# Performance work log

Measured on AMD Instinct MI355X. Metric: run time of the kernel, lower is better.

## Reference

```python
import jax, jax.numpy as jnp
import numpy as np
import math

D_MODEL = 1024
HEADS = 16
HEAD_DIM = D_MODEL // HEADS
B, S = 2, 2048


def setup_inputs() -> dict:
    key = jax.random.key(0)
    ks = jax.random.split(key, 7)
    scale = 1.0 / math.sqrt(D_MODEL)
    return {
        "query": jax.random.normal(ks[0], (B, S, D_MODEL), dtype=jnp.float32),
        "key": jax.random.normal(ks[1], (B, S, D_MODEL), dtype=jnp.float32),
        "value": jax.random.normal(ks[2], (B, S, D_MODEL), dtype=jnp.float32),
        # causal mask, broadcast over batch and heads: [1, 1, S, S]
        "mask": jnp.tril(jnp.ones((S, S), dtype=bool))[None, None],
        "Wq": jax.random.normal(ks[3], (D_MODEL, D_MODEL), dtype=jnp.float32) * scale,
        "Wk": jax.random.normal(ks[4], (D_MODEL, D_MODEL), dtype=jnp.float32) * scale,
        "Wv": jax.random.normal(ks[5], (D_MODEL, D_MODEL), dtype=jnp.float32) * scale,
        "Wo": jax.random.normal(ks[6], (D_MODEL, D_MODEL), dtype=jnp.float32) * scale,
    }


def reference(query, key, value, mask, Wq, Wk, Wv, Wo):
    # bias-free projections (nn.Linear: x @ W.T)
    q = query @ Wq.T  # [B, S, D]
    k = key @ Wk.T
    v = value @ Wv.T

    def split_heads(x):  # [B, S, D] -> [B, H, S, Dh]
        return x.reshape(B, -1, HEADS, HEAD_DIM).transpose(0, 2, 1, 3)

    q, k, v = split_heads(q), split_heads(k), split_heads(v)

    # scores: [B, H, S, S]
    scores = jnp.einsum("bhsd,bhtd->bhst", q, k) / math.sqrt(HEAD_DIM)
    scores = jnp.where(mask, scores, -1e9)
    attn = jax.nn.softmax(scores, axis=-1)
    # dropout omitted (eval-mode reference; p=0.1 in training)
    out = jnp.einsum("bhst,bhtd->bhsd", attn, v)  # [B, H, S, Dh]
    out = out.transpose(0, 2, 1, 3).reshape(B, -1, D_MODEL)
    return out @ Wo.T
```

## Files before the change

kernel.cpp:

```cpp
#include <hip/hip_runtime.h>

#define BATCH 2
#define SEQ   2048
#define DMODEL 1024
#define NHEADS 16
#define HDIM  64

typedef __attribute__((ext_vector_type(8))) short short8v;
typedef __attribute__((ext_vector_type(4))) float f32x4;
typedef unsigned int uint32;

__device__ __forceinline__ unsigned short bf16rne(float x) {
    uint32 u = __float_as_uint(x);
    return (unsigned short)((u + 0x7FFFu + ((u >> 16) & 1u)) >> 16);
}
__device__ __forceinline__ void split1(float x, unsigned short& h, unsigned short& l) {
    uint32 u = __float_as_uint(x);
    uint32 hb = (u + 0x7FFFu + ((u >> 16) & 1u)) & 0xFFFF0000u;
    h = (unsigned short)(hb >> 16);
    float r = x - __uint_as_float(hb);
    l = bf16rne(r);
}

__global__ __launch_bounds__(256)
void cvt_hi3(const float* __restrict__ s0, const float* __restrict__ s1,
             const float* __restrict__ s2, short* __restrict__ d0,
             short* __restrict__ d1, short* __restrict__ d2, int n) {
    const float* src; short* dst;
    if (blockIdx.y == 0)      { src = s0; dst = d0; }
    else if (blockIdx.y == 1) { src = s1; dst = d1; }
    else                      { src = s2; dst = d2; }
    int i = (blockIdx.x * 256 + threadIdx.x) * 4;
    if (i >= n) return;
    float4 x = *reinterpret_cast<const float4*>(src + i);
    *reinterpret_cast<ushort4*>(dst + i) =
        make_ushort4(bf16rne(x.x), bf16rne(x.y), bf16rne(x.z), bf16rne(x.w));
}

__global__ __launch_bounds__(256)
void split_hl(const float* __restrict__ src, short* __restrict__ hi,
              short* __restrict__ lo, int n) {
    int i = (blockIdx.x * 256 + threadIdx.x) * 4;
    if (i >= n) return;
    float4 x = *reinterpret_cast<const float4*>(src + i);
    unsigned short h0, h1, h2, h3, l0, l1, l2, l3;
    split1(x.x, h0, l0); split1(x.y, h1, l1);
    split1(x.z, h2, l2); split1(x.w, h3, l3);
    *reinterpret_cast<ushort4*>(hi + i) = make_ushort4(h0, h1, h2, h3);
    *reinterpret_cast<ushort4*>(lo + i) = make_ushort4(l0, l1, l2, l3);
}

__device__ __forceinline__ void gload_lds16(const void* g, void* l) {
    __builtin_amdgcn_global_load_lds((const __attribute__((address_space(1))) void*)g,
                                     (__attribute__((address_space(3))) void*)l,
                                     16, 0, 0);
}

__global__ __launch_bounds__(256)
void gemm_qkv_bf16(const short* __restrict__ aq, const short* __restrict__ ak,
                   const short* __restrict__ av,
                   const short* __restrict__ wq, const short* __restrict__ wk,
                   const short* __restrict__ wv,
                   short* __restrict__ qo, short* __restrict__ ko,
                   short* __restrict__ vo) {
    __shared__ short As[128 * 64];
    __shared__ short Bs[128 * 64];
    const int tid = threadIdx.x;
    const int lane = tid & 63;
    const int w = tid >> 6, wm = w >> 1, wn = w & 1;
    const int r = lane & 15, g = lane >> 4;

    int soff[4];
    #pragma unroll
    for (int c = 0; c < 4; ++c) {
        const int u = c * 256 + tid, row = u >> 3, s = u & 7;
        soff[c] = row * 1024 + ((s ^ (row & 7)) * 8);
    }

    const int z = blockIdx.z;
    const short* A; const short* B; int bm, bn;
    if (z == 0)      { A = aq; B = wq; bm = blockIdx.y * 128; bn = blockIdx.x * 128; }
    else if (z == 1) { A = ak; B = wk; bm = blockIdx.y * 128; bn = blockIdx.x * 128; }
    else             { A = wv; B = av; bm = blockIdx.x * 128; bn = blockIdx.y * 128; }

    f32x4 acc[4][4];
    #pragma unroll
    for (int i = 0; i < 4; ++i)
        #pragma unroll
        for (int j = 0; j < 4; ++j) acc[i][j] = (f32x4){0.f, 0.f, 0.f, 0.f};

    const short* Arow = A + (size_t)bm * 1024;
    const short* Brow = B + (size_t)bn * 1024;
    for (int k0 = 0; k0 < 1024; k0 += 64) {
        __syncthreads();
        #pragma unroll
        for (int c = 0; c < 4; ++c) {
            gload_lds16(Arow + k0 + soff[c], &As[(c * 256 + tid) * 8]);
            gload_lds16(Brow + k0 + soff[c], &Bs[(c * 256 + tid) * 8]);
        }
        __syncthreads();
        #pragma unroll
        for (int kk = 0; kk < 2; ++kk) {
            short8v af[4], bf[4];
            #pragma unroll
            for (int fm = 0; fm < 4; ++fm)
                af[fm] = *(const short8v*)&As[(wm * 64 + fm * 16 + r) * 64 +
                                              (((kk * 4 + g) ^ (r & 7))) * 8];
            #pragma unroll
            for (int fn = 0; fn < 4; ++fn)
                bf[fn] = *(const short8v*)&Bs[(wn * 64 + fn * 16 + r) * 64 +
                                              (((kk * 4 + g) ^ (r & 7))) * 8];
            #pragma unroll
            for (int fm = 0; fm < 4; ++fm)
                #pragma unroll
                for (int fn = 0; fn < 4; ++fn)
                    acc[fm][fn] = __builtin_amdgcn_mfma_f32_16x16x32_bf16(
                        af[fm], bf[fn], acc[fm][fn], 0, 0, 0);
        }
    }

    #pragma unroll
    for (int fm = 0; fm < 4; ++fm)
        #pragma unroll
        for (int fn = 0; fn < 4; ++fn)
            #pragma unroll
            for (int qi = 0; qi < 4; ++qi) {
                const int mrow = bm + wm * 64 + fm * 16 + g * 4 + qi;
                const int ncol = bn + wn * 64 + fn * 16 + r;
                const float v = acc[fm][fn][qi];
                if (z == 0) {
                    size_t idx = ((size_t)((mrow >> 11) * 16 + (ncol >> 6))) * (SEQ * 64)
                               + (size_t)(mrow & 2047) * 64 + (ncol & 63);
                    qo[idx] = (short)bf16rne(v * 0.125f);
                } else if (z == 1) {
                    size_t idx = ((size_t)((mrow >> 11) * 16 + (ncol >> 6))) * (SEQ * 64)
                               + (size_t)(mrow & 2047) * 64 + (ncol & 63);
                    ko[idx] = (short)bf16rne(v);
                } else {
                    size_t idx = ((size_t)((ncol >> 11) * 16 + (mrow >> 6))) * (SEQ * 64)
                               + (size_t)(mrow & 63) * SEQ + (ncol & 2047);
                    vo[idx] = (short)bf16rne(v);
                }
            }
}

__device__ __forceinline__ void gemm512_pass(const short* __restrict__ Arow,
                                             const short* __restrict__ Brow,
                                             short* As, short* Bs,
                                             f32x4 (&acc)[4][2], int tid) {
    const int lane = tid & 63;
    const int w = tid >> 6, wm = w >> 2, wn = w & 3;
    const int r = lane & 15, g = lane >> 4;
    int soff[2];
    #pragma unroll
    for (int c = 0; c < 2; ++c) {
        const int u = c * 512 + tid, row = u >> 3, s = u & 7;
        soff[c] = row * 1024 + ((s ^ (row & 7)) * 8);
    }
    for (int k0 = 0; k0 < 1024; k0 += 64) {
        __syncthreads();
        #pragma unroll
        for (int c = 0; c < 2; ++c) {
            gload_lds16(Arow + k0 + soff[c], &As[(c * 512 + tid) * 8]);
            gload_lds16(Brow + k0 + soff[c], &Bs[(c * 512 + tid) * 8]);
        }
        __syncthreads();
        #pragma unroll
        for (int kk = 0; kk < 2; ++kk) {
            short8v af[4], bf[2];
            #pragma unroll
            for (int fm = 0; fm < 4; ++fm)
                af[fm] = *(const short8v*)&As[(wm * 64 + fm * 16 + r) * 64 +
                                              (((kk * 4 + g) ^ (r & 7))) * 8];
            #pragma unroll
            for (int fn = 0; fn < 2; ++fn)
                bf[fn] = *(const short8v*)&Bs[(wn * 32 + fn * 16 + r) * 64 +
                                              (((kk * 4 + g) ^ (r & 7))) * 8];
            #pragma unroll
            for (int fm = 0; fm < 4; ++fm)
                #pragma unroll
                for (int fn = 0; fn < 2; ++fn)
                    acc[fm][fn] = __builtin_amdgcn_mfma_f32_16x16x32_bf16(
                        af[fm], bf[fn], acc[fm][fn], 0, 0, 0);
        }
    }
}

__global__ __launch_bounds__(512)
void gemm_out_f32(const short* __restrict__ Ah, const short* __restrict__ Al,
                  const short* __restrict__ Bh, const short* __restrict__ Bl,
                  float* __restrict__ C) {
    __shared__ short As[128 * 64];
    __shared__ short Bs[128 * 64];
    const int tid = threadIdx.x;
    const int bm = blockIdx.y * 128, bn = blockIdx.x * 128;

    f32x4 acc[4][2];
    #pragma unroll
    for (int i = 0; i < 4; ++i)
        #pragma unroll
        for (int j = 0; j < 2; ++j) acc[i][j] = (f32x4){0.f, 0.f, 0.f, 0.f};

    gemm512_pass(Ah + (size_t)bm * 1024, Bh + (size_t)bn * 1024, As, Bs, acc, tid);
    gemm512_pass(Ah + (size_t)bm * 1024, Bl + (size_t)bn * 1024, As, Bs, acc, tid);
    gemm512_pass(Al + (size_t)bm * 1024, Bh + (size_t)bn * 1024, As, Bs, acc, tid);

    const int lane = tid & 63;
    const int w = tid >> 6, wm = w >> 2, wn = w & 3;
    const int r = lane & 15, g = lane >> 4;
    #pragma unroll
    for (int fm = 0; fm < 4; ++fm)
        #pragma unroll
        for (int fn = 0; fn < 2; ++fn)
            #pragma unroll
            for (int qi = 0; qi < 4; ++qi) {
                const int mrow = bm + wm * 64 + fm * 16 + g * 4 + qi;
                const int ncol = bn + wn * 32 + fn * 16 + r;
                C[(size_t)mrow * DMODEL + ncol] = acc[fm][fn][qi];
            }
}

__global__ __launch_bounds__(256, 3)
void attn_split(const short* __restrict__ qh, const short* __restrict__ kh,
                const short* __restrict__ vt, short* __restrict__ oh,
                short* __restrict__ ol) {
    __shared__ short Pl[4][32 * 64];
    __shared__ float Ls[4][32];
    const int tid  = threadIdx.x;
    const int lane = tid & 63;
    const int wid  = tid >> 6;
    const int r = lane & 15;
    const int g = lane >> 4;
    const int c  = 63 - (int)blockIdx.x;
    const int bh = blockIdx.y;
    short* Pw = Pl[wid];
    float* Ob = reinterpret_cast<float*>(&Pl[0][0]);

    const short* qB = qh + (size_t)bh * SEQ * 64;
    const short* kB = kh + (size_t)bh * SEQ * 64;
    const short* vB = vt + (size_t)bh * 64 * SEQ;
    const int b = bh >> 4, h = bh & 15;
    const int q0 = c * 32;
    const int nt = (c + 2) >> 1;

    short8v qf[2][2];
    #pragma unroll
    for (int fm = 0; fm < 2; ++fm)
        #pragma unroll
        for (int kk = 0; kk < 2; ++kk)
            qf[fm][kk] = *(const short8v*)(qB + (size_t)(q0 + fm * 16 + r) * 64 +
                                           (kk * 4 + g) * 8);

    f32x4 oacc[2][4];
    float lsum[2][4];
    #pragma unroll
    for (int fm = 0; fm < 2; ++fm) {
        #pragma unroll
        for (int fd = 0; fd < 4; ++fd) oacc[fm][fd] = (f32x4){0.f, 0.f, 0.f, 0.f};
        #pragma unroll
        for (int qi = 0; qi < 4; ++qi) lsum[fm][qi] = 0.f;
    }

    for (int kt = wid; kt < nt; kt += 4) {
        f32x4 sacc[2][4];
        #pragma unroll
        for (int fm = 0; fm < 2; ++fm)
            #pragma unroll
            for (int fn = 0; fn < 4; ++fn) sacc[fm][fn] = (f32x4){0.f, 0.f, 0.f, 0.f};
        #pragma unroll
        for (int kk = 0; kk < 2; ++kk) {
            short8v kf[4];
            #pragma unroll
            for (int fn = 0; fn < 4; ++fn)
                kf[fn] = *(const short8v*)(kB + (size_t)(kt * 64 + fn * 16 + r) * 64 +
                                           (kk * 4 + g) * 8);
            #pragma unroll
            for (int fm = 0; fm < 2; ++fm)
                #pragma unroll
                for (int fn = 0; fn < 4; ++fn)
                    sacc[fm][fn] = __builtin_amdgcn_mfma_f32_16x16x32_bf16(
                        qf[fm][kk], kf[fn], sacc[fm][fn], 0, 0, 0);
        }

        if (kt == nt - 1) {
            #pragma unroll
            for (int fm = 0; fm < 2; ++fm)
                #pragma unroll
                for (int fn = 0; fn < 4; ++fn)
                    #pragma unroll
                    for (int qi = 0; qi < 4; ++qi) {
                        const int qg = q0 + fm * 16 + g * 4 + qi;
                        const int kg = kt * 64 + fn * 16 + r;
                        if (kg > qg) sacc[fm][fn][qi] = -1.0e30f;
                    }
        }

        #pragma unroll
        for (int fm = 0; fm < 2; ++fm)
            #pragma unroll
            for (int fn = 0; fn < 4; ++fn)
                #pragma unroll
                for (int qi = 0; qi < 4; ++qi) {
                    const float p = __expf(sacc[fm][fn][qi]);
                    sacc[fm][fn][qi] = p;
                    lsum[fm][qi] += p;
                }

        #pragma unroll
        for (int fm = 0; fm < 2; ++fm)
            #pragma unroll
            for (int fn = 0; fn < 4; ++fn)
                #pragma unroll
                for (int qi = 0; qi < 4; ++qi) {
                    const int ql = fm * 16 + g * 4 + qi;
                    const int kl = fn * 16 + r;
                    Pw[ql * 64 + (((kl >> 3) ^ (ql & 7)) << 3) + (kl & 7)] =
                        (short)bf16rne(sacc[fm][fn][qi]);
                }

        #pragma unroll
        for (int kk = 0; kk < 2; ++kk) {
            short8v pf[2], vf[4];
            #pragma unroll
            for (int fm = 0; fm < 2; ++fm)
                pf[fm] = *(const short8v*)&Pw[(fm * 16 + r) * 64 +
                                              (((kk * 4 + g) ^ (r & 7))) * 8];
            #pragma unroll
            for (int fd = 0; fd < 4; ++fd)
                vf[fd] = *(const short8v*)(vB + (size_t)(fd * 16 + r) * SEQ +
                                           kt * 64 + (kk * 4 + g) * 8);
            #pragma unroll
            for (int fm = 0; fm < 2; ++fm)
                #pragma unroll
                for (int fd = 0; fd < 4; ++fd)
                    oacc[fm][fd] = __builtin_amdgcn_mfma_f32_16x16x32_bf16(
                        pf[fm], vf[fd], oacc[fm][fd], 0, 0, 0);
        }
    }

    #pragma unroll
    for (int fm = 0; fm < 2; ++fm)
        #pragma unroll
        for (int qi = 0; qi < 4; ++qi) {
            float s = lsum[fm][qi];
            s += __shfl_xor(s, 1);
            s += __shfl_xor(s, 2);
            s += __shfl_xor(s, 4);
            s += __shfl_xor(s, 8);
            lsum[fm][qi] = s;
        }
    if (r == 0) {
        #pragma unroll
        for (int fm = 0; fm < 2; ++fm)
            #pragma unroll
            for (int qi = 0; qi < 4; ++qi)
                Ls[wid][fm * 16 + g * 4 + qi] = lsum[fm][qi];
    }

    __syncthreads();

    if (wid >= 2) {
        float* dst = Ob + (wid - 2) * 2048;
        #pragma unroll
        for (int fm = 0; fm < 2; ++fm)
            #pragma unroll
            for (int fd = 0; fd < 4; ++fd)
                #pragma unroll
                for (int qi = 0; qi < 4; ++qi)
                    dst[(fm * 16 + g * 4 + qi) * 64 + fd * 16 + r] = oacc[fm][fd][qi];
    }
    __syncthreads();
    if (wid < 2) {
        const float* src = Ob + wid * 2048;
        #pragma unroll
        for (int fm = 0; fm < 2; ++fm)
            #pragma unroll
            for (int fd = 0; fd < 4; ++fd)
                #pragma unroll
                for (int qi = 0; qi < 4; ++qi)
                    oacc[fm][fd][qi] += src[(fm * 16 + g * 4 + qi) * 64 + fd * 16 + r];
    }
    __syncthreads();
    if (wid == 1) {
        #pragma unroll
        for (int fm = 0; fm < 2; ++fm)
            #pragma unroll
            for (int fd = 0; fd < 4; ++fd)
                #pragma unroll
                for (int qi = 0; qi < 4; ++qi)
                    Ob[(fm * 16 + g * 4 + qi) * 64 + fd * 16 + r] = oacc[fm][fd][qi];
    }
    __syncthreads();
    if (wid == 0) {
        #pragma unroll
        for (int fm = 0; fm < 2; ++fm)
            #pragma unroll
            for (int fd = 0; fd < 4; ++fd)
                #pragma unroll
                for (int qi = 0; qi < 4; ++qi)
                    oacc[fm][fd][qi] += Ob[(fm * 16 + g * 4 + qi) * 64 + fd * 16 + r];

        float inv[2][4];
        #pragma unroll
        for (int fm = 0; fm < 2; ++fm)
            #pragma unroll
            for (int qi = 0; qi < 4; ++qi) {
                const int row = fm * 16 + g * 4 + qi;
                inv[fm][qi] = 1.0f / (Ls[0][row] + Ls[1][row] + Ls[2][row] + Ls[3][row]);
            }

        #pragma unroll
        for (int fm = 0; fm < 2; ++fm)
            #pragma unroll
            for (int fd = 0; fd < 4; ++fd)
                #pragma unroll
                for (int qi = 0; qi < 4; ++qi) {
                    const float v = oacc[fm][fd][qi] * inv[fm][qi];
                    unsigned short hh, ll;
                    split1(v, hh, ll);
                    const int mg = b * SEQ + q0 + fm * 16 + g * 4 + qi;
                    const int nc = h * 64 + fd * 16 + r;
                    const size_t idx = (size_t)mg * DMODEL + nc;
                    oh[idx] = (short)hh; ol[idx] = (short)ll;
                }
    }
}

extern "C" void kernel_launch(void* const* d_in, const int* in_sizes, int n_in,
                              void* d_out, int out_size, void* d_ws, size_t ws_size,
                              hipStream_t stream) {
    const float* query = (const float*)d_in[0];
    const float* key   = (const float*)d_in[1];
    const float* value = (const float*)d_in[2];
    const float* Wq = (const float*)d_in[4];
    const float* Wk = (const float*)d_in[5];
    const float* Wv = (const float*)d_in[6];
    const float* Wo = (const float*)d_in[7];
    float* out = (float*)d_out;

    const size_t SD = (size_t)BATCH * SEQ * DMODEL;
    const size_t DD = (size_t)DMODEL * DMODEL;
    const int M = BATCH * SEQ;

    short* ws  = (short*)d_ws;
    short* aq  = ws;
    short* ak  = aq + SD;
    short* av  = ak + SD;
    short* wqh = av + SD;
    short* wkh = wqh + DD;
    short* wvh = wkh + DD;
    short* qh_ = wvh + DD;
    short* kh_ = qh_ + SD;
    short* vt_ = kh_ + SD;
    short* woh = vt_ + SD;
    short* wol = woh + DD;
    short* oh_ = aq;
    short* ol_ = ak;

    dim3 gc_a((unsigned)(SD / 1024), 3);
    cvt_hi3<<<gc_a, 256, 0, stream>>>(query, key, value, aq, ak, av, (int)SD);
    dim3 gc_w((unsigned)(DD / 1024), 3);
    cvt_hi3<<<gc_w, 256, 0, stream>>>(Wq, Wk, Wv, wqh, wkh, wvh, (int)DD);

    dim3 gq(DMODEL / 128, M / 128, 3);
    gemm_qkv_bf16<<<gq, 256, 0, stream>>>(aq, ak, av, wqh, wkh, wvh, qh_, kh_, vt_);

    dim3 ga(64, BATCH * NHEADS);
    attn_split<<<ga, 256, 0, stream>>>(qh_, kh_, vt_, oh_, ol_);

    split_hl<<<(int)(DD / 1024), 256, 0, stream>>>(Wo, woh, wol, (int)DD);

    dim3 go(DMODEL / 128, M / 128);
    gemm_out_f32<<<go, 512, 0, stream>>>(oh_, ol_, woh, wol, out);
}
```

Before: 329.4 us.

## Pair causal query chunks per block and switch softmax exponent to exp2

Each attention block now handles two query chunks, c and 63-c, so every block gets roughly the same causal workload and the grid is halved. Occupancy is raised to 4 blocks per CU, and the first V fragment load is issued before the masking and exp work to hide its latency. The Q projection scale now folds in log2(e), so the softmax can use the hardware exp2 instead of __expf. The catch is more barriers per block, and, as in the code before, no running max is subtracted, which relies on scores staying bounded.

```diff
diff --git a/kernel.cpp b/kernel.cpp
--- a/kernel.cpp
+++ b/kernel.cpp
@@ -20,6 +20,13 @@
     h = (unsigned short)(hb >> 16);
     float r = x - __uint_as_float(hb);
     l = bf16rne(r);
+}
+__device__ __forceinline__ float fexp2(float x) {
+#if __has_builtin(__builtin_amdgcn_exp2f)
+    return __builtin_amdgcn_exp2f(x);
+#else
+    return exp2f(x);
+#endif
 }
 
 __global__ __launch_bounds__(256)
@@ -131,7 +138,7 @@
                 if (z == 0) {
                     size_t idx = ((size_t)((mrow >> 11) * 16 + (ncol >> 6))) * (SEQ * 64)
                                + (size_t)(mrow & 2047) * 64 + (ncol & 63);
-                    qo[idx] = (short)bf16rne(v * 0.125f);
+                    qo[idx] = (short)bf16rne(v * 0.18033688011112043f);
                 } else if (z == 1) {
                     size_t idx = ((size_t)((mrow >> 11) * 16 + (ncol >> 6))) * (SEQ * 64)
                                + (size_t)(mrow & 2047) * 64 + (ncol & 63);
@@ -220,10 +227,10 @@
             }
 }
 
-__global__ __launch_bounds__(256, 3)
-void attn_split(const short* __restrict__ qh, const short* __restrict__ kh,
-                const short* __restrict__ vt, short* __restrict__ oh,
-                short* __restrict__ ol) {
+__global__ __launch_bounds__(256, 4)
+void attn_pair(const short* __restrict__ qh, const short* __restrict__ kh,
+               const short* __restrict__ vt, short* __restrict__ oh,
+               short* __restrict__ ol) {
     __shared__ short Pl[4][32 * 64];
     __shared__ float Ls[4][32];
     const int tid  = threadIdx.x;
@@ -231,7 +238,7 @@
     const int wid  = tid >> 6;
     const int r = lane & 15;
     const int g = lane >> 4;
-    const int c  = 63 - (int)blockIdx.x;
+    const int x  = blockIdx.x;
     const int bh = blockIdx.y;
     short* Pw = Pl[wid];
     float* Ob = reinterpret_cast<float*>(&Pl[0][0]);
@@ -240,189 +247,212 @@
     const short* kB = kh + (size_t)bh * SEQ * 64;
     const short* vB = vt + (size_t)bh * 64 * SEQ;
     const int b = bh >> 4, h = bh & 15;
-    const int q0 = c * 32;
-    const int nt = (c + 2) >> 1;
-
-    short8v qf[2][2];
-    #pragma unroll
-    for (int fm = 0; fm < 2; ++fm)
-        #pragma unroll
-        for (int kk = 0; kk < 2; ++kk)
-            qf[fm][kk] = *(const short8v*)(qB + (size_t)(q0 + fm * 16 + r) * 64 +
-                                           (kk * 4 + g) * 8);
-
-    f32x4 oacc[2][4];
-    float lsum[2][4];
-    #pragma unroll
-    for (int fm = 0; fm < 2; ++fm) {
-        #pragma unroll
-        for (int fd = 0; fd < 4; ++fd) oacc[fm][fd] = (f32x4){0.f, 0.f, 0.f, 0.f};
-        #pragma unroll
-        for (int qi = 0; qi < 4; ++qi) lsum[fm][qi] = 0.f;
-    }
-
-    for (int kt = wid; kt < nt; kt += 4) {
-        f32x4 sacc[2][4];
+
+    #pragma unroll
+    for (int half = 0; half < 2; ++half) {
+        const int c  = half ? (63 - x) : x;
+        const int q0 = c * 32;
+        const int nt = (c + 2) >> 1;
+
+        short8v qf[2][2];
         #pragma unroll
         for (int fm = 0; fm < 2; ++fm)
             #pragma unroll
-            for (int fn = 0; fn < 4; ++fn) sacc[fm][fn] = (f32x4){0.f, 0.f, 0.f, 0.f};
-        #pragma unroll
-        for (int kk = 0; kk < 2; ++kk) {
-            short8v kf[4];
-            #pragma unroll
-            for (int fn = 0; fn < 4; ++fn)
-                kf[fn] = *(const short8v*)(kB + (size_t)(kt * 64 + fn * 16 + r) * 64 +
-                                           (kk * 4 + g) * 8);
-            #pragma unroll
-            for (int fm = 0; fm < 2; ++fm)
+            for (int kk = 0; kk < 2; ++kk)
+                qf[fm][kk] = *(const short8v*)(qB + (size_t)(q0 + fm * 16 + r) * 64 +
+                                               (kk * 4 + g) * 8);
+
+        f32x4 oacc[2][4];
+        float lsum[2][4];
+        #pragma unroll
+        for (int fm = 0; fm < 2; ++fm) {
+            #pragma unroll
+            for (int fd = 0; fd < 4; ++fd) oacc[fm][fd] = (f32x4){0.f, 0.f, 0.f, 0.f};
+            #pragma unroll
+            for (int qi = 0; qi < 4; ++qi) lsum[fm][qi] = 0.f;
+        }
+
+        for (int kt = wid; kt < nt; kt += 4) {
+            f32x4 sacc[2][4];
+            #pragma unroll
+            for (int fm = 0; fm < 2; ++fm)
+                #pragma unroll
+                for (int fn = 0; fn < 4; ++fn) sacc[fm][fn] = (f32x4){0.f, 0.f, 0.f, 0.f};
+            #pragma unroll
+            for (int kk = 0; kk < 2; ++kk) {
+                short8v kf[4];
                 #pragma unroll
                 for (int fn = 0; fn < 4; ++fn)
-                    sacc[fm][fn] = __builtin_amdgcn_mfma_f32_16x16x32_bf16(
-                        qf[fm][kk], kf[fn], sacc[fm][fn], 0, 0, 0);
-        }
-
-        if (kt == nt - 1) {
+                    kf[fn] = *(const short8v*)(kB + (size_t)(kt * 64 + fn * 16 + r) * 64 +
+                                               (kk * 4 + g) * 8);
+                #pragma unroll
+                for (int fm = 0; fm < 2; ++fm)
+                    #pragma unroll
+                    for (int fn = 0; fn < 4; ++fn)
+                        sacc[fm][fn] = __builtin_amdgcn_mfma_f32_16x16x32_bf16(
+                            qf[fm][kk], kf[fn], sacc[fm][fn], 0, 0, 0);
+            }
+
+            short8v vf0[4];
+            #pragma unroll
+            for (int fd = 0; fd < 4; ++fd)
+                vf0[fd] = *(const short8v*)(vB + (size_t)(fd * 16 + r) * SEQ +
+                                            kt * 64 + g * 8);
+
+            if (kt == nt - 1) {
+                #pragma unroll
+                for (int fm = 0; fm < 2; ++fm)
+                    #pragma unroll
+                    for (int fn = 0; fn < 4; ++fn)
+                        #pragma unroll
+                        for (int qi = 0; qi < 4; ++qi) {
+                            const int qg = q0 + fm * 16 + g * 4 + qi;
+                            const int kg = kt * 64 + fn * 16 + r;
+                            if (kg > qg) sacc[fm][fn][qi] = -1.0e30f;
+                        }
+            }
+
             #pragma unroll
             for (int fm = 0; fm < 2; ++fm)
                 #pragma unroll
                 for (int fn = 0; fn < 4; ++fn)
                     #pragma unroll
                     for (int qi = 0; qi < 4; ++qi) {
-                        const int qg = q0 + fm * 16 + g * 4 + qi;
-                        const int kg = kt * 64 + fn * 16 + r;
-                        if (kg > qg) sacc[fm][fn][qi] = -1.0e30f;
+                        const float p = fexp2(sacc[fm][fn][qi]);
+                        sacc[fm][fn][qi] = p;
+                        lsum[fm][qi] += p;
                     }
+
+            #pragma unroll
+            for (int fm = 0; fm < 2; ++fm)
+                #pragma unroll
+                for (int fn = 0; fn < 4; ++fn)
+                    #pragma unroll
+                    for (int qi = 0; qi < 4; ++qi) {
+                        const int ql = fm * 16 + g * 4 + qi;
+                        const int kl = fn * 16 + r;
+                        Pw[ql * 64 + (((kl >> 3) ^ (ql & 7)) << 3) + (kl & 7)] =
+                            (short)bf16rne(sacc[fm][fn][qi]);
+                    }
+
+            {
+                short8v pf[2];
+                #pragma unroll
+                for (int fm = 0; fm < 2; ++fm)
+                    pf[fm] = *(const short8v*)&Pw[(fm * 16 + r) * 64 +
+                                                  ((g ^ (r & 7))) * 8];
+                #pragma unroll
+                for (int fm = 0; fm < 2; ++fm)
+                    #pragma unroll
+                    for (int fd = 0; fd < 4; ++fd)
+                        oacc[fm][fd] = __builtin_amdgcn_mfma_f32_16x16x32_bf16(
+                            pf[fm], vf0[fd], oacc[fm][fd], 0, 0, 0);
+            }
+            {
+                short8v pf[2], vf1[4];
+                #pragma unroll
+                for (int fd = 0; fd < 4; ++fd)
+                    vf1[fd] = *(const short8v*)(vB + (size_t)(fd * 16 + r) * SEQ +
+                                                kt * 64 + (4 + g) * 8);
+                #pragma unroll
+                for (int fm = 0; fm < 2; ++fm)
+                    pf[fm] = *(const short8v*)&Pw[(fm * 16 + r) * 64 +
+                                                  (((4 + g) ^ (r & 7))) * 8];
+                #pragma unroll
+                for (int fm = 0; fm < 2; ++fm)
+                    #pragma unroll
+                    for (int fd = 0; fd < 4; ++fd)
+                        oacc[fm][fd] = __builtin_amdgcn_mfma_f32_16x16x32_bf16(
+                            pf[fm], vf1[fd], oacc[fm][fd], 0, 0, 0);
+            }
         }
 
         #pragma unroll
         for (int fm = 0; fm < 2; ++fm)
             #pragma unroll
-            for (int fn = 0; fn < 4; ++fn)
+            for (int qi = 0; qi < 4; ++qi) {
+                float s = lsum[fm][qi];
+                s += __shfl_xor(s, 1);
+                s += __shfl_xor(s, 2);
+                s += __shfl_xor(s, 4);
+                s += __shfl_xor(s, 8);
+                lsum[fm][qi] = s;
+            }
+        if (r == 0) {
+            #pragma unroll
+            for (int fm = 0; fm < 2; ++fm)
+                #pragma unroll
+                for (int qi = 0; qi < 4; ++qi)
+                    Ls[wid][fm * 16 + g * 4 + qi] = lsum[fm][qi];
+        }
+
+        __syncthreads();
+        if (wid >= 2) {
+            float* dst = Ob + (wid - 2) * 2048;
+            #pragma unroll
+            for (int fm = 0; fm < 2; ++fm)
+                #pragma unroll
+                for (int fd = 0; fd < 4; ++fd)
+                    #pragma unroll
+                    for (int qi = 0; qi < 4; ++qi)
+                        dst[(fm * 16 + g * 4 + qi) * 64 + fd * 16 + r] = oacc[fm][fd][qi];
+        }
+        __syncthreads();
+        if (wid < 2) {
+            const float* src = Ob + wid * 2048;
+            #pragma unroll
+            for (int fm = 0; fm < 2; ++fm)
+                #pragma unroll
+                for (int fd = 0; fd < 4; ++fd)
+                    #pragma unroll
+                    for (int qi = 0; qi < 4; ++qi)
+                        oacc[fm][fd][qi] += src[(fm * 16 + g * 4 + qi) * 64 + fd * 16 + r];
+        }
+        __syncthreads();
+        if (wid == 1) {
+            #pragma unroll
+            for (int fm = 0; fm < 2; ++fm)
+                #pragma unroll
+                for (int fd = 0; fd < 4; ++fd)
+                    #pragma unroll
+                    for (int qi = 0; qi < 4; ++qi)
+                        Ob[(fm * 16 + g * 4 + qi) * 64 + fd * 16 + r] = oacc[fm][fd][qi];
+        }
+        __syncthreads();
+        float inv[2][4];
+        if (wid == 0) {
+            #pragma unroll
+            for (int fm = 0; fm < 2; ++fm)
+                #pragma unroll
+                for (int fd = 0; fd < 4; ++fd)
+                    #pragma unroll
+                    for (int qi = 0; qi < 4; ++qi)
+                        oacc[fm][fd][qi] += Ob[(fm * 16 + g * 4 + qi) * 64 + fd * 16 + r];
+            #pragma unroll
+            for (int fm = 0; fm < 2; ++fm)
                 #pragma unroll
                 for (int qi = 0; qi < 4; ++qi) {
-                    const float p = __expf(sacc[fm][fn][qi]);
-                    sacc[fm][fn][qi] = p;
-                    lsum[fm][qi] += p;
+                    const int row = fm * 16 + g * 4 + qi;
+                    inv[fm][qi] = 1.0f / (Ls[0][row] + Ls[1][row] + Ls[2][row] + Ls[3][row]);
                 }
-
-        #pragma unroll
-        for (int fm = 0; fm < 2; ++fm)
-            #pragma unroll
-            for (int fn = 0; fn < 4; ++fn)
-                #pragma unroll
-                for (int qi = 0; qi < 4; ++qi) {
-                    const int ql = fm * 16 + g * 4 + qi;
-                    const int kl = fn * 16 + r;
-                    Pw[ql * 64 + (((kl >> 3) ^ (ql & 7)) << 3) + (kl & 7)] =
-                        (short)bf16rne(sacc[fm][fn][qi]);
-                }
-
-        #pragma unroll
-        for (int kk = 0; kk < 2; ++kk) {
-            short8v pf[2], vf[4];
-            #pragma unroll
-            for (int fm = 0; fm < 2; ++fm)
-                pf[fm] = *(const short8v*)&Pw[(fm * 16 + r) * 64 +
-                                              (((kk * 4 + g) ^ (r & 7))) * 8];
-            #pragma unroll
-            for (int fd = 0; fd < 4; ++fd)
-                vf[fd] = *(const short8v*)(vB + (size_t)(fd * 16 + r) * SEQ +
-                                           kt * 64 + (kk * 4 + g) * 8);
+        }
+        __syncthreads();
+        if (wid == 0) {
             #pragma unroll
             for (int fm = 0; fm < 2; ++fm)
                 #pragma unroll
                 for (int fd = 0; fd < 4; ++fd)
-                    oacc[fm][fd] = __builtin_amdgcn_mfma_f32_16x16x32_bf16(
-                        pf[fm], vf[fd], oacc[fm][fd], 0, 0, 0);
-        }
-    }
-
-    #pragma unroll
-    for (int fm = 0; fm < 2; ++fm)
-        #pragma unroll
-        for (int qi = 0; qi < 4; ++qi) {
-            float s = lsum[fm][qi];
-            s += __shfl_xor(s, 1);
-            s += __shfl_xor(s, 2);
-            s += __shfl_xor(s, 4);
-            s += __shfl_xor(s, 8);
-            lsum[fm][qi] = s;
-        }
-    if (r == 0) {
-        #pragma unroll
-        for (int fm = 0; fm < 2; ++fm)
-            #pragma unroll
-            for (int qi = 0; qi < 4; ++qi)
-                Ls[wid][fm * 16 + g * 4 + qi] = lsum[fm][qi];
-    }
-
-    __syncthreads();
-
-    if (wid >= 2) {
-        float* dst = Ob + (wid - 2) * 2048;
-        #pragma unroll
-        for (int fm = 0; fm < 2; ++fm)
-            #pragma unroll
-            for (int fd = 0; fd < 4; ++fd)
-                #pragma unroll
-                for (int qi = 0; qi < 4; ++qi)
-                    dst[(fm * 16 + g * 4 + qi) * 64 + fd * 16 + r] = oacc[fm][fd][qi];
-    }
-    __syncthreads();
-    if (wid < 2) {
-        const float* src = Ob + wid * 2048;
-        #pragma unroll
-        for (int fm = 0; fm < 2; ++fm)
-            #pragma unroll
-            for (int fd = 0; fd < 4; ++fd)
-                #pragma unroll
-                for (int qi = 0; qi < 4; ++qi)
-                    oacc[fm][fd][qi] += src[(fm * 16 + g * 4 + qi) * 64 + fd * 16 + r];
-    }
-    __syncthreads();
-    if (wid == 1) {
-        #pragma unroll
-        for (int fm = 0; fm < 2; ++fm)
-            #pragma unroll
-            for (int fd = 0; fd < 4; ++fd)
-                #pragma unroll
-                for (int qi = 0; qi < 4; ++qi)
-                    Ob[(fm * 16 + g * 4 + qi) * 64 + fd * 16 + r] = oacc[fm][fd][qi];
-    }
-    __syncthreads();
-    if (wid == 0) {
-        #pragma unroll
-        for (int fm = 0; fm < 2; ++fm)
-            #pragma unroll
-            for (int fd = 0; fd < 4; ++fd)
-                #pragma unroll
-                for (int qi = 0; qi < 4; ++qi)
-                    oacc[fm][fd][qi] += Ob[(fm * 16 + g * 4 + qi) * 64 + fd * 16 + r];
-
-        float inv[2][4];
-        #pragma unroll
-        for (int fm = 0; fm < 2; ++fm)
-            #pragma unroll
-            for (int qi = 0; qi < 4; ++qi) {
-                const int row = fm * 16 + g * 4 + qi;
-                inv[fm][qi] = 1.0f / (Ls[0][row] + Ls[1][row] + Ls[2][row] + Ls[3][row]);
-            }
-
-        #pragma unroll
-        for (int fm = 0; fm < 2; ++fm)
-            #pragma unroll
-            for (int fd = 0; fd < 4; ++fd)
-                #pragma unroll
-                for (int qi = 0; qi < 4; ++qi) {
-                    const float v = oacc[fm][fd][qi] * inv[fm][qi];
-                    unsigned short hh, ll;
-                    split1(v, hh, ll);
-                    const int mg = b * SEQ + q0 + fm * 16 + g * 4 + qi;
-                    const int nc = h * 64 + fd * 16 + r;
-                    const size_t idx = (size_t)mg * DMODEL + nc;
-                    oh[idx] = (short)hh; ol[idx] = (short)ll;
-                }
+                    #pragma unroll
+                    for (int qi = 0; qi < 4; ++qi) {
+                        const float v = oacc[fm][fd][qi] * inv[fm][qi];
+                        unsigned short hh, ll;
+                        split1(v, hh, ll);
+                        const int mg = b * SEQ + q0 + fm * 16 + g * 4 + qi;
+                        const int nc = h * 64 + fd * 16 + r;
+                        const size_t idx = (size_t)mg * DMODEL + nc;
+                        oh[idx] = (short)hh; ol[idx] = (short)ll;
+                    }
+        }
     }
 }
 
@@ -465,8 +495,8 @@
     dim3 gq(DMODEL / 128, M / 128, 3);
     gemm_qkv_bf16<<<gq, 256, 0, stream>>>(aq, ak, av, wqh, wkh, wvh, qh_, kh_, vt_);
 
-    dim3 ga(64, BATCH * NHEADS);
-    attn_split<<<ga, 256, 0, stream>>>(qh_, kh_, vt_, oh_, ol_);
+    dim3 ga(32, BATCH * NHEADS);
+    attn_pair<<<ga, 256, 0, stream>>>(qh_, kh_, vt_, oh_, ol_);
 
     split_hl<<<(int)(DD / 1024), 256, 0, stream>>>(Wo, woh, wol, (int)DD);
 
```

Result: slower. 396.1 us (+20.3%).
